# Kernel tuning notes

Hardware: AMD Instinct MI355X
Metric: run time of the kernel (lower is better)

Reference implementation:

```python
import jax, jax.numpy as jnp
import numpy as np

D_MODEL, N_HEAD, N_KV_HEAD, D_HEAD = 1024, 16, 4, 64


def rotate_half(x):
    x1, x2 = x[..., : x.shape[-1] // 2], x[..., x.shape[-1] // 2:]
    return jnp.concatenate((-x2, x1), axis=-1)


def rope_cos_sin(seq_len, dim, dtype=jnp.float32):
    inv_freq = 1.0 / (10000.0 ** (jnp.arange(0, dim, 2, dtype=jnp.float32) / dim))
    t = jnp.arange(seq_len, dtype=jnp.float32)
    freqs = jnp.einsum('i,j->ij', t, inv_freq)          # [S, dim/2]
    emb = jnp.concatenate((freqs, freqs), axis=-1)       # [S, dim]
    return jnp.cos(emb).astype(dtype), jnp.sin(emb).astype(dtype)


def setup_inputs() -> dict:
    key = jax.random.key(0)
    ks = jax.random.split(key, 5)
    B, S = 2, 2048
    scale = 0.02
    return {
        'x': jax.random.normal(ks[0], (B, S, D_MODEL), dtype=jnp.float32),
        'Wq': jax.random.normal(ks[1], (D_MODEL, N_HEAD * D_HEAD), dtype=jnp.float32) * scale,
        'Wk': jax.random.normal(ks[2], (D_MODEL, N_KV_HEAD * D_HEAD), dtype=jnp.float32) * scale,
        'Wv': jax.random.normal(ks[3], (D_MODEL, N_KV_HEAD * D_HEAD), dtype=jnp.float32) * scale,
        'Wo': jax.random.normal(ks[4], (N_HEAD * D_HEAD, D_MODEL), dtype=jnp.float32) * scale,
    }


def reference(x, Wq, Wk, Wv, Wo):
    B, S, _ = x.shape
    scale = 1.0 / np.sqrt(D_HEAD)
    # projections -> [B, H, S, Dh]
    q = (x @ Wq).reshape(B, S, N_HEAD, D_HEAD).transpose(0, 2, 1, 3)
    k = (x @ Wk).reshape(B, S, N_KV_HEAD, D_HEAD).transpose(0, 2, 1, 3)
    v = (x @ Wv).reshape(B, S, N_KV_HEAD, D_HEAD).transpose(0, 2, 1, 3)
    cos, sin = rope_cos_sin(S, D_HEAD, x.dtype)          # [S, Dh]
    q = q * cos + rotate_half(q) * sin
    k = k * cos + rotate_half(k) * sin
    rep = N_HEAD // N_KV_HEAD
    k = jnp.repeat(k, rep, axis=1)                       # [B, H, S, Dh]
    v = jnp.repeat(v, rep, axis=1)
    scores = jnp.einsum('bhqd,bhkd->bhqk', q, k) * scale # [B, H, S, S]
    causal = jnp.triu(jnp.ones((S, S), dtype=bool), k=1)
    scores = jnp.where(causal, -jnp.inf, scores)
    probs = jax.nn.softmax(scores, axis=-1)
    ctx = jnp.einsum('bhqk,bhkd->bhqd', probs, v)        # [B, H, S, Dh]
    ctx = ctx.transpose(0, 2, 1, 3).reshape(B, S, N_HEAD * D_HEAD)
    return ctx @ Wo
```

## Files before the change

kernel.cpp:

```cpp
#include <hip/hip_runtime.h>
#include <hip/hip_bf16.h>
#include <cstdint>
#include <math.h>

#define S_LEN 2048
#define DM 1024
#define NQKV 1536
#define MROWS 4096

typedef __attribute__((ext_vector_type(8))) short short8;
typedef __attribute__((ext_vector_type(4))) short short4v;
typedef __attribute__((ext_vector_type(4))) float f32x4;

#define MEMBAR() __asm__ __volatile__("" ::: "memory")

#define QFOLD 0.18033688011112042f

__device__ __forceinline__ short f2bf(float x) {
  union { float f; uint32_t u; } v; v.f = x;
  uint32_t r = (v.u + 0x7fffu + ((v.u >> 16) & 1u)) >> 16;
  return (short)(uint16_t)r;
}

__device__ __forceinline__ uint32_t pk2(float a, float b) {
  __hip_bfloat162 h = __float22bfloat162_rn(make_float2(a, b));
  union { __hip_bfloat162 h2; uint32_t u; } cv; cv.h2 = h;
  return cv.u;
}

__global__ void f32_to_bf16_vec(const float* __restrict__ in, short* __restrict__ out, int n4) {
  int i = blockIdx.x * blockDim.x + threadIdx.x;
  if (i < n4) {
    float4 v = ((const float4*)in)[i];
    short4 o;
    o.x = f2bf(v.x); o.y = f2bf(v.y); o.z = f2bf(v.z); o.w = f2bf(v.w);
    ((short4*)out)[i] = o;
  }
}

__global__ __launch_bounds__(256) void transpose_f32_bf16(const float* __restrict__ src,
    short* __restrict__ dst, int R, int C) {
  __shared__ short T[64 * 72];
  const int r0 = blockIdx.x * 64, c0 = blockIdx.y * 64;
  const int tid = threadIdx.x;
  #pragma unroll
  for (int i = 0; i < 4; ++i) {
    int chunk = tid + i * 256;
    int r = chunk >> 4, cc = (chunk & 15) * 4;
    float4 v = *(const float4*)&src[(size_t)(r0 + r) * C + c0 + cc];
    T[(cc + 0) * 72 + r] = f2bf(v.x);
    T[(cc + 1) * 72 + r] = f2bf(v.y);
    T[(cc + 2) * 72 + r] = f2bf(v.z);
    T[(cc + 3) * 72 + r] = f2bf(v.w);
  }
  __syncthreads();
  #pragma unroll
  for (int i = 0; i < 2; ++i) {
    int chunk = tid + i * 256;
    int rr = chunk >> 3, kk = (chunk & 7) * 8;
    *(uint4*)&dst[(size_t)(c0 + rr) * R + r0 + kk] = *(uint4*)&T[rr * 72 + kk];
  }
}

#define BM 128
#define BN 128
#define BKT 64
#define LDT 72

__global__ __launch_bounds__(256) void gemm_bf16(const short* __restrict__ A,
    const short* __restrict__ BT, float* __restrict__ C, int M, int N, int K) {
  __shared__ short As[BM * LDT];
  __shared__ short Bs[BN * LDT];
  const int tid = threadIdx.x;
  const int wave = tid >> 6, lane = tid & 63;
  const int quad = lane >> 4, l15 = lane & 15;
  const int wm = (wave >> 1) * 64, wn = (wave & 1) * 64;
  const int m0 = blockIdx.y * BM, n0 = blockIdx.x * BN;

  f32x4 acc[4][4] = {};

  for (int k0 = 0; k0 < K; k0 += BKT) {
    __syncthreads();
    #pragma unroll
    for (int i = 0; i < 4; ++i) {
      int chunk = tid + i * 256;
      int r = chunk >> 3, c = (chunk & 7) * 8;
      *(uint4*)&As[r*LDT + c] = *(const uint4*)&A[(size_t)(m0 + r)*K + k0 + c];
      *(uint4*)&Bs[r*LDT + c] = *(const uint4*)&BT[(size_t)(n0 + r)*K + k0 + c];
    }
    __syncthreads();
    #pragma unroll
    for (int ks = 0; ks < 2; ++ks) {
      short8 af[4], bfr[4];
      #pragma unroll
      for (int mi = 0; mi < 4; ++mi)
        af[mi] = *(const short8*)&As[(wm + mi*16 + l15)*LDT + ks*32 + quad*8];
      #pragma unroll
      for (int ni = 0; ni < 4; ++ni)
        bfr[ni] = *(const short8*)&Bs[(wn + ni*16 + l15)*LDT + ks*32 + quad*8];
      #pragma unroll
      for (int mi = 0; mi < 4; ++mi)
        #pragma unroll
        for (int ni = 0; ni < 4; ++ni)
          acc[mi][ni] = __builtin_amdgcn_mfma_f32_16x16x32_bf16(af[mi], bfr[ni], acc[mi][ni], 0, 0, 0);
    }
  }
  #pragma unroll
  for (int mi = 0; mi < 4; ++mi)
    #pragma unroll
    for (int ni = 0; ni < 4; ++ni)
      #pragma unroll
      for (int r = 0; r < 4; ++r)
        C[(size_t)(m0 + wm + mi*16 + quad*4 + r)*N + (n0 + wn + ni*16 + l15)] = acc[mi][ni][r];
}

__global__ void rope_kernel(const float* __restrict__ qkv, short* __restrict__ Qb,
                            short* __restrict__ Kb, short* __restrict__ Vb) {
  __shared__ float csn[64];
  const int row = blockIdx.x;
  const int s = row & (S_LEN - 1);
  const int tid = threadIdx.x;
  const float* rp = qkv + (size_t)row * NQKV;
  if (tid < 32) {
    float inv = exp2f(-(float)tid * 0.41524101186092029f);
    float ang = (float)s * inv;
    csn[tid] = cosf(ang);
    csn[tid + 32] = sinf(ang);
  }
  __syncthreads();
  #pragma unroll
  for (int i = 0; i < 2; ++i) {
    int p = tid + i * 256;
    int hh = p >> 5, j = p & 31;
    float cs = csn[j], sn = csn[j + 32];
    float x1 = rp[hh*64 + j], x2 = rp[hh*64 + j + 32];
    Qb[(size_t)row*1024 + hh*64 + j]      = f2bf((x1*cs - x2*sn) * QFOLD);
    Qb[(size_t)row*1024 + hh*64 + j + 32] = f2bf((x2*cs + x1*sn) * QFOLD);
  }
  if (tid < 128) {
    int hh = tid >> 5, j = tid & 31;
    float cs = csn[j], sn = csn[j + 32];
    float x1 = rp[1024 + hh*64 + j], x2 = rp[1024 + hh*64 + j + 32];
    Kb[(size_t)row*256 + hh*64 + j]      = f2bf(x1*cs - x2*sn);
    Kb[(size_t)row*256 + hh*64 + j + 32] = f2bf(x2*cs + x1*sn);
  }
  Vb[(size_t)row*256 + tid] = f2bf(rp[1280 + tid]);
}

__global__ __launch_bounds__(256) void transpose_v(const short* __restrict__ Vb,
                                                   short* __restrict__ Vt) {
  __shared__ short T[64 * 72];
  const int s0 = blockIdx.x * 64;
  const int bh = blockIdx.y;
  const int b = bh >> 2, kvh = bh & 3;
  const int tid = threadIdx.x;
  #pragma unroll
  for (int i = 0; i < 2; ++i) {
    int chunk = tid + i * 256;
    int r = chunk >> 3, c = (chunk & 7) * 8;
    short8 v = *(const short8*)&Vb[(size_t)(b*S_LEN + s0 + r)*256 + kvh*64 + c];
    #pragma unroll
    for (int t = 0; t < 8; ++t) T[(c + t) * 72 + r] = v[t];
  }
  __syncthreads();
  #pragma unroll
  for (int i = 0; i < 2; ++i) {
    int chunk = tid + i * 256;
    int rr = chunk >> 3, kk = (chunk & 7) * 8;
    *(uint4*)&Vt[(size_t)(bh*64 + rr)*S_LEN + s0 + kk] = *(uint4*)&T[rr * 72 + kk];
  }
}

#define PSTR 136

__global__ __launch_bounds__(256, 2) void fattn3(const short* __restrict__ Qb,
    const short* __restrict__ Kb, const short* __restrict__ Vt, short* __restrict__ Ctx) {
  __shared__ short Ks[128 * 72];
  __shared__ short Vts[64 * PSTR];
  __shared__ short Ps[4 * 32 * PSTR];
  __shared__ float Asc[4 * 32];
  const int idx = blockIdx.x;
  const int pair = idx & 255;
  const int j   = pair & 15;
  const int hh  = (pair >> 4) & 1;
  const int kvh = (pair >> 5) & 3;
  const int b   = pair >> 7;
  const int jt  = (idx < 256) ? j : (31 - j);
  const int q0  = jt * 64;
  const int ntiles = (jt >> 1) + 1;
  const int tid = threadIdx.x, wave = tid >> 6, lane = tid & 63;
  const int quad = lane >> 4, l15 = lane & 15;
  const int h    = kvh*4 + hh*2 + (wave >> 1);
  const int roff = (wave & 1) * 32;
  const size_t qbase  = (size_t)b * S_LEN * 1024;
  const size_t kbase  = (size_t)b * S_LEN * 256;
  const size_t vtbase = (size_t)(b*4 + kvh) * 64 * S_LEN;
  short* Psw = Ps + wave * 32 * PSTR;
  float* AscW = Asc + wave * 32;

  short8 qf[2][2];
  #pragma unroll
  for (int mi = 0; mi < 2; ++mi)
    #pragma unroll
    for (int ks = 0; ks < 2; ++ks)
      qf[mi][ks] = *(const short8*)&Qb[qbase + (size_t)(q0 + roff + mi*16 + l15)*1024
                                       + h*64 + ks*32 + quad*8];

  f32x4 O[2][4] = {};
  float mm[2] = {-INFINITY, -INFINITY};
  float ll[2] = {0.f, 0.f};

  short8 kreg[4], vreg[4];
  #pragma unroll
  for (int i = 0; i < 4; ++i) {
    int chunk = tid + i * 256;
    int kr = chunk >> 3, kc = (chunk & 7) * 8;
    kreg[i] = *(const short8*)&Kb[kbase + (size_t)kr*256 + kvh*64 + kc];
    int vr = chunk >> 4, vc = (chunk & 15) * 8;
    vreg[i] = *(const short8*)&Vt[vtbase + (size_t)vr*S_LEN + vc];
  }

  for (int t = 0; t < ntiles; ++t) {
    const int k0 = t * 128;
    __syncthreads();
    #pragma unroll
    for (int i = 0; i < 4; ++i) {
      int chunk = tid + i * 256;
      int kr = chunk >> 3, kc = (chunk & 7) * 8;
      *(short8*)&Ks[kr*72 + kc] = kreg[i];
      int vr = chunk >> 4, vc = (chunk & 15) * 8;
      *(short8*)&Vts[vr*PSTR + vc] = vreg[i];
    }
    __syncthreads();
    if (t + 1 < ntiles) {
      const int kn = (t + 1) * 128;
      #pragma unroll
      for (int i = 0; i < 4; ++i) {
        int chunk = tid + i * 256;
        int kr = chunk >> 3, kc = (chunk & 7) * 8;
        kreg[i] = *(const short8*)&Kb[kbase + (size_t)(kn + kr)*256 + kvh*64 + kc];
        int vr = chunk >> 4, vc = (chunk & 15) * 8;
        vreg[i] = *(const short8*)&Vt[vtbase + (size_t)vr*S_LEN + kn + vc];
      }
    }

    f32x4 sc[2][8];
    #pragma unroll
    for (int nt = 0; nt < 8; ++nt) {
      short8 k0f = *(const short8*)&Ks[(nt*16 + l15)*72 + quad*8];
      short8 k1f = *(const short8*)&Ks[(nt*16 + l15)*72 + 32 + quad*8];
      #pragma unroll
      for (int mi = 0; mi < 2; ++mi) {
        f32x4 acc = {0.f, 0.f, 0.f, 0.f};
        acc = __builtin_amdgcn_mfma_f32_16x16x32_bf16(k0f, qf[mi][0], acc, 0, 0, 0);
        acc = __builtin_amdgcn_mfma_f32_16x16x32_bf16(k1f, qf[mi][1], acc, 0, 0, 0);
        sc[mi][nt] = acc;
      }
    }

    const bool lastt = (t == ntiles - 1);
    float al[2];
    #pragma unroll
    for (int mi = 0; mi < 2; ++mi) {
      const int qrow = q0 + roff + mi*16 + l15;
      if (lastt) {
        #pragma unroll
        for (int nt = 0; nt < 8; ++nt)
          #pragma unroll
          for (int r = 0; r < 4; ++r)
            if (k0 + nt*16 + quad*4 + r > qrow) sc[mi][nt][r] = -1e30f;
      }
      float mx = -1e30f;
      #pragma unroll
      for (int nt = 0; nt < 8; ++nt) {
        float a = fmaxf(sc[mi][nt][0], sc[mi][nt][1]);
        float c = fmaxf(sc[mi][nt][2], sc[mi][nt][3]);
        mx = fmaxf(mx, fmaxf(a, c));
      }
      mx = fmaxf(mx, __shfl_xor(mx, 16, 64));
      mx = fmaxf(mx, __shfl_xor(mx, 32, 64));
      float mn = fmaxf(mm[mi], mx);
      float alpha = exp2f(mm[mi] - mn);
      float sum = 0.f;
      #pragma unroll
      for (int nt = 0; nt < 8; ++nt) {
        float p0 = exp2f(sc[mi][nt][0] - mn);
        float p1 = exp2f(sc[mi][nt][1] - mn);
        float p2 = exp2f(sc[mi][nt][2] - mn);
        float p3 = exp2f(sc[mi][nt][3] - mn);
        sum += (p0 + p1) + (p2 + p3);
        union { uint2 u; short4v s; } pkc;
        pkc.u.x = pk2(p0, p1); pkc.u.y = pk2(p2, p3);
        *(short4v*)&Psw[(mi*16 + l15)*PSTR + nt*16 + quad*4] = pkc.s;
      }
      sum += __shfl_xor(sum, 16, 64);
      sum += __shfl_xor(sum, 32, 64);
      ll[mi] = ll[mi]*alpha + sum;
      mm[mi] = mn;
      al[mi] = alpha;
    }
    if (quad < 2) AscW[quad*16 + l15] = al[quad];
    MEMBAR();
    float av0[4], av1[4];
    #pragma unroll
    for (int r = 0; r < 4; ++r) {
      av0[r] = AscW[quad*4 + r];
      av1[r] = AscW[16 + quad*4 + r];
    }
    #pragma unroll
    for (int d = 0; d < 4; ++d)
      #pragma unroll
      for (int r = 0; r < 4; ++r) {
        O[0][d][r] *= av0[r];
        O[1][d][r] *= av1[r];
      }

    #pragma unroll
    for (int ks = 0; ks < 4; ++ks) {
      short8 a0 = *(const short8*)&Psw[(0*16 + l15)*PSTR + ks*32 + quad*8];
      short8 a1 = *(const short8*)&Psw[(1*16 + l15)*PSTR + ks*32 + quad*8];
      #pragma unroll
      for (int d = 0; d < 4; ++d) {
        short8 bv = *(const short8*)&Vts[(d*16 + l15)*PSTR + ks*32 + quad*8];
        O[0][d] = __builtin_amdgcn_mfma_f32_16x16x32_bf16(a0, bv, O[0][d], 0, 0, 0);
        O[1][d] = __builtin_amdgcn_mfma_f32_16x16x32_bf16(a1, bv, O[1][d], 0, 0, 0);
      }
    }
  }

  if (quad < 2) AscW[quad*16 + l15] = 1.0f / ll[quad];
  MEMBAR();
  float lv0[4], lv1[4];
  #pragma unroll
  for (int r = 0; r < 4; ++r) {
    lv0[r] = AscW[quad*4 + r];
    lv1[r] = AscW[16 + quad*4 + r];
  }
  #pragma unroll
  for (int d = 0; d < 4; ++d)
    #pragma unroll
    for (int r = 0; r < 4; ++r) {
      int qrow0 = q0 + roff + quad*4 + r;
      Ctx[qbase + (size_t)qrow0*1024 + h*64 + d*16 + l15] = f2bf(O[0][d][r] * lv0[r]);
      int qrow1 = q0 + roff + 16 + quad*4 + r;
      Ctx[qbase + (size_t)qrow1*1024 + h*64 + d*16 + l15] = f2bf(O[1][d][r] * lv1[r]);
    }
}

extern "C" void kernel_launch(void* const* d_in, const int* in_sizes, int n_in,
                              void* d_out, int out_size, void* d_ws, size_t ws_size,
                              hipStream_t stream) {
  const float* x  = (const float*)d_in[0];
  const float* Wq = (const float*)d_in[1];
  const float* Wk = (const float*)d_in[2];
  const float* Wv = (const float*)d_in[3];
  const float* Wo = (const float*)d_in[4];
  float* out = (float*)d_out;

  char* w = (char*)d_ws;
  short* Xb    = (short*)w;  w += (size_t)MROWS * DM * 2;
  short* WcatT = (short*)w;  w += (size_t)NQKV * DM * 2;
  short* WoT   = (short*)w;  w += (size_t)DM * DM * 2;
  float* QKVf  = (float*)w;  w += (size_t)MROWS * NQKV * 4;
  short* Qbuf  = (short*)w;  w += (size_t)MROWS * DM * 2;
  short* Kbuf  = (short*)w;  w += (size_t)MROWS * 256 * 2;
  short* Vbuf  = (short*)w;  w += (size_t)MROWS * 256 * 2;
  short* Vt    = (short*)w;  w += (size_t)8 * 64 * S_LEN * 2;
  short* Ctx   = (short*)QKVf;

  f32_to_bf16_vec<<<dim3(4096), dim3(256), 0, stream>>>(x, Xb, MROWS * DM / 4);
  transpose_f32_bf16<<<dim3(16, 16), dim3(256), 0, stream>>>(Wq, WcatT, 1024, 1024);
  transpose_f32_bf16<<<dim3(16, 4),  dim3(256), 0, stream>>>(Wk, WcatT + (size_t)1024*1024, 1024, 256);
  transpose_f32_bf16<<<dim3(16, 4),  dim3(256), 0, stream>>>(Wv, WcatT + (size_t)1280*1024, 1024, 256);
  transpose_f32_bf16<<<dim3(16, 16), dim3(256), 0, stream>>>(Wo, WoT, 1024, 1024);

  gemm_bf16<<<dim3(NQKV / BN, MROWS / BM), dim3(256), 0, stream>>>(Xb, WcatT, QKVf, MROWS, NQKV, DM);
  rope_kernel<<<dim3(MROWS), dim3(256), 0, stream>>>(QKVf, Qbuf, Kbuf, Vbuf);
  transpose_v<<<dim3(32, 8), dim3(256), 0, stream>>>(Vbuf, Vt);
  fattn3<<<dim3(512), dim3(256), 0, stream>>>(Qbuf, Kbuf, Vt, Ctx);
  gemm_bf16<<<dim3(DM / BN, MROWS / BM), dim3(256), 0, stream>>>(Ctx, WoT, out, MROWS, DM, DM);
}
```

Before: 198.1 us.

## Use direct global-to-LDS loads in GEMM and pair causal tiles per attention block

The GEMM tile staging switches from register round-trips to global_load_lds direct copies into an unpadded LDS layout, reducing VGPR traffic and instructions per load. The attention kernel now launches one block per head-pair group that processes query tile j and its mirror 31-j sequentially, giving 256 equally loaded blocks with one block per CU. The unpadded LDS stride may introduce bank conflicts on fragment reads, and serial processing of two tiles removes the latency hiding that two resident blocks per CU used to provide.

```diff
diff --git a/kernel.cpp b/kernel.cpp
--- a/kernel.cpp
+++ b/kernel.cpp
@@ -65,28 +65,35 @@
 #define BM 128
 #define BN 128
 #define BKT 64
-#define LDT 72
 
 __global__ __launch_bounds__(256) void gemm_bf16(const short* __restrict__ A,
     const short* __restrict__ BT, float* __restrict__ C, int M, int N, int K) {
-  __shared__ short As[BM * LDT];
-  __shared__ short Bs[BN * LDT];
+  __shared__ short As[BM * BKT];
+  __shared__ short Bs[BN * BKT];
   const int tid = threadIdx.x;
   const int wave = tid >> 6, lane = tid & 63;
   const int quad = lane >> 4, l15 = lane & 15;
   const int wm = (wave >> 1) * 64, wn = (wave & 1) * 64;
   const int m0 = blockIdx.y * BM, n0 = blockIdx.x * BN;
 
+  const int sr = wave * 32 + (lane >> 3);
+  const int scol = (lane & 7) * 8;
+
   f32x4 acc[4][4] = {};
 
   for (int k0 = 0; k0 < K; k0 += BKT) {
     __syncthreads();
     #pragma unroll
-    for (int i = 0; i < 4; ++i) {
-      int chunk = tid + i * 256;
-      int r = chunk >> 3, c = (chunk & 7) * 8;
-      *(uint4*)&As[r*LDT + c] = *(const uint4*)&A[(size_t)(m0 + r)*K + k0 + c];
-      *(uint4*)&Bs[r*LDT + c] = *(const uint4*)&BT[(size_t)(n0 + r)*K + k0 + c];
+    for (int j = 0; j < 4; ++j) {
+      const int r = sr + j * 8;
+      __builtin_amdgcn_global_load_lds(
+          (const __attribute__((address_space(1))) void*)&A[(size_t)(m0 + r) * K + k0 + scol],
+          (__attribute__((address_space(3))) void*)&As[(wave * 4 + j) * 512],
+          16, 0, 0);
+      __builtin_amdgcn_global_load_lds(
+          (const __attribute__((address_space(1))) void*)&BT[(size_t)(n0 + r) * K + k0 + scol],
+          (__attribute__((address_space(3))) void*)&Bs[(wave * 4 + j) * 512],
+          16, 0, 0);
     }
     __syncthreads();
     #pragma unroll
@@ -94,10 +101,10 @@
       short8 af[4], bfr[4];
       #pragma unroll
       for (int mi = 0; mi < 4; ++mi)
-        af[mi] = *(const short8*)&As[(wm + mi*16 + l15)*LDT + ks*32 + quad*8];
+        af[mi] = *(const short8*)&As[(wm + mi*16 + l15)*BKT + ks*32 + quad*8];
       #pragma unroll
       for (int ni = 0; ni < 4; ++ni)
-        bfr[ni] = *(const short8*)&Bs[(wn + ni*16 + l15)*LDT + ks*32 + quad*8];
+        bfr[ni] = *(const short8*)&Bs[(wn + ni*16 + l15)*BKT + ks*32 + quad*8];
       #pragma unroll
       for (int mi = 0; mi < 4; ++mi)
         #pragma unroll
@@ -173,21 +180,17 @@
 
 #define PSTR 136
 
-__global__ __launch_bounds__(256, 2) void fattn3(const short* __restrict__ Qb,
+__global__ __launch_bounds__(256, 1) void fattn4(const short* __restrict__ Qb,
     const short* __restrict__ Kb, const short* __restrict__ Vt, short* __restrict__ Ctx) {
   __shared__ short Ks[128 * 72];
   __shared__ short Vts[64 * PSTR];
   __shared__ short Ps[4 * 32 * PSTR];
   __shared__ float Asc[4 * 32];
   const int idx = blockIdx.x;
-  const int pair = idx & 255;
-  const int j   = pair & 15;
-  const int hh  = (pair >> 4) & 1;
-  const int kvh = (pair >> 5) & 3;
-  const int b   = pair >> 7;
-  const int jt  = (idx < 256) ? j : (31 - j);
-  const int q0  = jt * 64;
-  const int ntiles = (jt >> 1) + 1;
+  const int j   = idx & 15;
+  const int hh  = (idx >> 4) & 1;
+  const int kvh = (idx >> 5) & 3;
+  const int b   = idx >> 7;
   const int tid = threadIdx.x, wave = tid >> 6, lane = tid & 63;
   const int quad = lane >> 4, l15 = lane & 15;
   const int h    = kvh*4 + hh*2 + (wave >> 1);
@@ -198,153 +201,159 @@
   short* Psw = Ps + wave * 32 * PSTR;
   float* AscW = Asc + wave * 32;
 
-  short8 qf[2][2];
-  #pragma unroll
-  for (int mi = 0; mi < 2; ++mi)
-    #pragma unroll
-    for (int ks = 0; ks < 2; ++ks)
-      qf[mi][ks] = *(const short8*)&Qb[qbase + (size_t)(q0 + roff + mi*16 + l15)*1024
-                                       + h*64 + ks*32 + quad*8];
-
-  f32x4 O[2][4] = {};
-  float mm[2] = {-INFINITY, -INFINITY};
-  float ll[2] = {0.f, 0.f};
-
-  short8 kreg[4], vreg[4];
-  #pragma unroll
-  for (int i = 0; i < 4; ++i) {
-    int chunk = tid + i * 256;
-    int kr = chunk >> 3, kc = (chunk & 7) * 8;
-    kreg[i] = *(const short8*)&Kb[kbase + (size_t)kr*256 + kvh*64 + kc];
-    int vr = chunk >> 4, vc = (chunk & 15) * 8;
-    vreg[i] = *(const short8*)&Vt[vtbase + (size_t)vr*S_LEN + vc];
-  }
-
-  for (int t = 0; t < ntiles; ++t) {
-    const int k0 = t * 128;
-    __syncthreads();
+  for (int half = 0; half < 2; ++half) {
+    const int jt = half ? (31 - j) : j;
+    const int q0 = jt * 64;
+    const int ntiles = (jt >> 1) + 1;
+
+    short8 qf[2][2];
+    #pragma unroll
+    for (int mi = 0; mi < 2; ++mi)
+      #pragma unroll
+      for (int ks = 0; ks < 2; ++ks)
+        qf[mi][ks] = *(const short8*)&Qb[qbase + (size_t)(q0 + roff + mi*16 + l15)*1024
+                                         + h*64 + ks*32 + quad*8];
+
+    f32x4 O[2][4] = {};
+    float mm[2] = {-INFINITY, -INFINITY};
+    float ll[2] = {0.f, 0.f};
+
+    short8 kreg[4], vreg[4];
     #pragma unroll
     for (int i = 0; i < 4; ++i) {
       int chunk = tid + i * 256;
       int kr = chunk >> 3, kc = (chunk & 7) * 8;
-      *(short8*)&Ks[kr*72 + kc] = kreg[i];
+      kreg[i] = *(const short8*)&Kb[kbase + (size_t)kr*256 + kvh*64 + kc];
       int vr = chunk >> 4, vc = (chunk & 15) * 8;
-      *(short8*)&Vts[vr*PSTR + vc] = vreg[i];
-    }
-    __syncthreads();
-    if (t + 1 < ntiles) {
-      const int kn = (t + 1) * 128;
+      vreg[i] = *(const short8*)&Vt[vtbase + (size_t)vr*S_LEN + vc];
+    }
+
+    for (int t = 0; t < ntiles; ++t) {
+      const int k0 = t * 128;
+      __syncthreads();
       #pragma unroll
       for (int i = 0; i < 4; ++i) {
         int chunk = tid + i * 256;
         int kr = chunk >> 3, kc = (chunk & 7) * 8;
-        kreg[i] = *(const short8*)&Kb[kbase + (size_t)(kn + kr)*256 + kvh*64 + kc];
+        *(short8*)&Ks[kr*72 + kc] = kreg[i];
         int vr = chunk >> 4, vc = (chunk & 15) * 8;
-        vreg[i] = *(const short8*)&Vt[vtbase + (size_t)vr*S_LEN + kn + vc];
-      }
-    }
-
-    f32x4 sc[2][8];
-    #pragma unroll
-    for (int nt = 0; nt < 8; ++nt) {
-      short8 k0f = *(const short8*)&Ks[(nt*16 + l15)*72 + quad*8];
-      short8 k1f = *(const short8*)&Ks[(nt*16 + l15)*72 + 32 + quad*8];
+        *(short8*)&Vts[vr*PSTR + vc] = vreg[i];
+      }
+      __syncthreads();
+      if (t + 1 < ntiles) {
+        const int kn = (t + 1) * 128;
+        #pragma unroll
+        for (int i = 0; i < 4; ++i) {
+          int chunk = tid + i * 256;
+          int kr = chunk >> 3, kc = (chunk & 7) * 8;
+          kreg[i] = *(const short8*)&Kb[kbase + (size_t)(kn + kr)*256 + kvh*64 + kc];
+          int vr = chunk >> 4, vc = (chunk & 15) * 8;
+          vreg[i] = *(const short8*)&Vt[vtbase + (size_t)vr*S_LEN + kn + vc];
+        }
+      }
+
+      f32x4 sc[2][8];
+      #pragma unroll
+      for (int nt = 0; nt < 8; ++nt) {
+        short8 k0f = *(const short8*)&Ks[(nt*16 + l15)*72 + quad*8];
+        short8 k1f = *(const short8*)&Ks[(nt*16 + l15)*72 + 32 + quad*8];
+        #pragma unroll
+        for (int mi = 0; mi < 2; ++mi) {
+          f32x4 acc = {0.f, 0.f, 0.f, 0.f};
+          acc = __builtin_amdgcn_mfma_f32_16x16x32_bf16(k0f, qf[mi][0], acc, 0, 0, 0);
+          acc = __builtin_amdgcn_mfma_f32_16x16x32_bf16(k1f, qf[mi][1], acc, 0, 0, 0);
+          sc[mi][nt] = acc;
+        }
+      }
+
+      const bool lastt = (t == ntiles - 1);
+      float al[2];
       #pragma unroll
       for (int mi = 0; mi < 2; ++mi) {
-        f32x4 acc = {0.f, 0.f, 0.f, 0.f};
-        acc = __builtin_amdgcn_mfma_f32_16x16x32_bf16(k0f, qf[mi][0], acc, 0, 0, 0);
-        acc = __builtin_amdgcn_mfma_f32_16x16x32_bf16(k1f, qf[mi][1], acc, 0, 0, 0);
-        sc[mi][nt] = acc;
-      }
-    }
-
-    const bool lastt = (t == ntiles - 1);
-    float al[2];
-    #pragma unroll
-    for (int mi = 0; mi < 2; ++mi) {
-      const int qrow = q0 + roff + mi*16 + l15;
-      if (lastt) {
-        #pragma unroll
-        for (int nt = 0; nt < 8; ++nt)
+        const int qrow = q0 + roff + mi*16 + l15;
+        if (lastt) {
           #pragma unroll
-          for (int r = 0; r < 4; ++r)
-            if (k0 + nt*16 + quad*4 + r > qrow) sc[mi][nt][r] = -1e30f;
-      }
-      float mx = -1e30f;
-      #pragma unroll
-      for (int nt = 0; nt < 8; ++nt) {
-        float a = fmaxf(sc[mi][nt][0], sc[mi][nt][1]);
-        float c = fmaxf(sc[mi][nt][2], sc[mi][nt][3]);
-        mx = fmaxf(mx, fmaxf(a, c));
-      }
-      mx = fmaxf(mx, __shfl_xor(mx, 16, 64));
-      mx = fmaxf(mx, __shfl_xor(mx, 32, 64));
-      float mn = fmaxf(mm[mi], mx);
-      float alpha = exp2f(mm[mi] - mn);
-      float sum = 0.f;
-      #pragma unroll
-      for (int nt = 0; nt < 8; ++nt) {
-        float p0 = exp2f(sc[mi][nt][0] - mn);
-        float p1 = exp2f(sc[mi][nt][1] - mn);
-        float p2 = exp2f(sc[mi][nt][2] - mn);
-        float p3 = exp2f(sc[mi][nt][3] - mn);
-        sum += (p0 + p1) + (p2 + p3);
-        union { uint2 u; short4v s; } pkc;
-        pkc.u.x = pk2(p0, p1); pkc.u.y = pk2(p2, p3);
-        *(short4v*)&Psw[(mi*16 + l15)*PSTR + nt*16 + quad*4] = pkc.s;
-      }
-      sum += __shfl_xor(sum, 16, 64);
-      sum += __shfl_xor(sum, 32, 64);
-      ll[mi] = ll[mi]*alpha + sum;
-      mm[mi] = mn;
-      al[mi] = alpha;
-    }
-    if (quad < 2) AscW[quad*16 + l15] = al[quad];
+          for (int nt = 0; nt < 8; ++nt)
+            #pragma unroll
+            for (int r = 0; r < 4; ++r)
+              if (k0 + nt*16 + quad*4 + r > qrow) sc[mi][nt][r] = -1e30f;
+        }
+        float mx = -1e30f;
+        #pragma unroll
+        for (int nt = 0; nt < 8; ++nt) {
+          float a = fmaxf(sc[mi][nt][0], sc[mi][nt][1]);
+          float c = fmaxf(sc[mi][nt][2], sc[mi][nt][3]);
+          mx = fmaxf(mx, fmaxf(a, c));
+        }
+        mx = fmaxf(mx, __shfl_xor(mx, 16, 64));
+        mx = fmaxf(mx, __shfl_xor(mx, 32, 64));
+        float mn = fmaxf(mm[mi], mx);
+        float alpha = exp2f(mm[mi] - mn);
+        float sum = 0.f;
+        #pragma unroll
+        for (int nt = 0; nt < 8; ++nt) {
+          float p0 = exp2f(sc[mi][nt][0] - mn);
+          float p1 = exp2f(sc[mi][nt][1] - mn);
+          float p2 = exp2f(sc[mi][nt][2] - mn);
+          float p3 = exp2f(sc[mi][nt][3] - mn);
+          sum += (p0 + p1) + (p2 + p3);
+          union { uint2 u; short4v s; } pkc;
+          pkc.u.x = pk2(p0, p1); pkc.u.y = pk2(p2, p3);
+          *(short4v*)&Psw[(mi*16 + l15)*PSTR + nt*16 + quad*4] = pkc.s;
+        }
+        sum += __shfl_xor(sum, 16, 64);
+        sum += __shfl_xor(sum, 32, 64);
+        ll[mi] = ll[mi]*alpha + sum;
+        mm[mi] = mn;
+        al[mi] = alpha;
+      }
+      if (quad < 2) AscW[quad*16 + l15] = al[quad];
+      MEMBAR();
+      float av0[4], av1[4];
+      #pragma unroll
+      for (int r = 0; r < 4; ++r) {
+        av0[r] = AscW[quad*4 + r];
+        av1[r] = AscW[16 + quad*4 + r];
+      }
+      #pragma unroll
+      for (int d = 0; d < 4; ++d)
+        #pragma unroll
+        for (int r = 0; r < 4; ++r) {
+          O[0][d][r] *= av0[r];
+          O[1][d][r] *= av1[r];
+        }
+
+      #pragma unroll
+      for (int ks = 0; ks < 4; ++ks) {
+        short8 a0 = *(const short8*)&Psw[(0*16 + l15)*PSTR + ks*32 + quad*8];
+        short8 a1 = *(const short8*)&Psw[(1*16 + l15)*PSTR + ks*32 + quad*8];
+        #pragma unroll
+        for (int d = 0; d < 4; ++d) {
+          short8 bv = *(const short8*)&Vts[(d*16 + l15)*PSTR + ks*32 + quad*8];
+          O[0][d] = __builtin_amdgcn_mfma_f32_16x16x32_bf16(a0, bv, O[0][d], 0, 0, 0);
+          O[1][d] = __builtin_amdgcn_mfma_f32_16x16x32_bf16(a1, bv, O[1][d], 0, 0, 0);
+        }
+      }
+    }
+
+    if (quad < 2) AscW[quad*16 + l15] = 1.0f / ll[quad];
     MEMBAR();
-    float av0[4], av1[4];
+    float lv0[4], lv1[4];
     #pragma unroll
     for (int r = 0; r < 4; ++r) {
-      av0[r] = AscW[quad*4 + r];
-      av1[r] = AscW[16 + quad*4 + r];
+      lv0[r] = AscW[quad*4 + r];
+      lv1[r] = AscW[16 + quad*4 + r];
     }
     #pragma unroll
     for (int d = 0; d < 4; ++d)
       #pragma unroll
       for (int r = 0; r < 4; ++r) {
-        O[0][d][r] *= av0[r];
-        O[1][d][r] *= av1[r];
-      }
-
-    #pragma unroll
-    for (int ks = 0; ks < 4; ++ks) {
-      short8 a0 = *(const short8*)&Psw[(0*16 + l15)*PSTR + ks*32 + quad*8];
-      short8 a1 = *(const short8*)&Psw[(1*16 + l15)*PSTR + ks*32 + quad*8];
-      #pragma unroll
-      for (int d = 0; d < 4; ++d) {
-        short8 bv = *(const short8*)&Vts[(d*16 + l15)*PSTR + ks*32 + quad*8];
-        O[0][d] = __builtin_amdgcn_mfma_f32_16x16x32_bf16(a0, bv, O[0][d], 0, 0, 0);
-        O[1][d] = __builtin_amdgcn_mfma_f32_16x16x32_bf16(a1, bv, O[1][d], 0, 0, 0);
-      }
-    }
-  }
-
-  if (quad < 2) AscW[quad*16 + l15] = 1.0f / ll[quad];
-  MEMBAR();
-  float lv0[4], lv1[4];
-  #pragma unroll
-  for (int r = 0; r < 4; ++r) {
-    lv0[r] = AscW[quad*4 + r];
-    lv1[r] = AscW[16 + quad*4 + r];
-  }
-  #pragma unroll
-  for (int d = 0; d < 4; ++d)
-    #pragma unroll
-    for (int r = 0; r < 4; ++r) {
-      int qrow0 = q0 + roff + quad*4 + r;
-      Ctx[qbase + (size_t)qrow0*1024 + h*64 + d*16 + l15] = f2bf(O[0][d][r] * lv0[r]);
-      int qrow1 = q0 + roff + 16 + quad*4 + r;
-      Ctx[qbase + (size_t)qrow1*1024 + h*64 + d*16 + l15] = f2bf(O[1][d][r] * lv1[r]);
-    }
+        int qrow0 = q0 + roff + quad*4 + r;
+        Ctx[qbase + (size_t)qrow0*1024 + h*64 + d*16 + l15] = f2bf(O[0][d][r] * lv0[r]);
+        int qrow1 = q0 + roff + 16 + quad*4 + r;
+        Ctx[qbase + (size_t)qrow1*1024 + h*64 + d*16 + l15] = f2bf(O[1][d][r] * lv1[r]);
+      }
+  }
 }
 
 extern "C" void kernel_launch(void* const* d_in, const int* in_sizes, int n_in,
@@ -377,6 +386,6 @@
   gemm_bf16<<<dim3(NQKV / BN, MROWS / BM), dim3(256), 0, stream>>>(Xb, WcatT, QKVf, MROWS, NQKV, DM);
   rope_kernel<<<dim3(MROWS), dim3(256), 0, stream>>>(QKVf, Qbuf, Kbuf, Vbuf);
   transpose_v<<<dim3(32, 8), dim3(256), 0, stream>>>(Vbuf, Vt);
-  fattn3<<<dim3(512), dim3(256), 0, stream>>>(Qbuf, Kbuf, Vt, Ctx);
+  fattn4<<<dim3(256), dim3(256), 0, stream>>>(Qbuf, Kbuf, Vt, Ctx);
   gemm_bf16<<<dim3(DM / BN, MROWS / BM), dim3(256), 0, stream>>>(Ctx, WoT, out, MROWS, DM, DM);
 }
```

Result: slower. 219.2 us (+10.6%).
